# Kernel tuning notes

Measured on AMD Instinct MI355X. Metric: run time of the kernel, lower is better.

The kernel has to match this reference:

```python
import jax, jax.numpy as jnp
import numpy as np

C, CL = 64, 8
N_PTS, GRID = 250_000, 160
G2 = GRID // 2


def _build():
    """Build sparse coords and MinkowskiEngine-style kernel maps (numpy, int constants)."""
    rng = np.random.default_rng(0)
    raw = rng.integers(0, GRID, size=(int(N_PTS * 1.3), 3))
    keys = (raw[:, 0] * GRID + raw[:, 1]) * GRID + raw[:, 2]
    _, uidx = np.unique(keys, return_index=True)
    coords = raw[np.sort(uidx)][:N_PTS]
    n_in = coords.shape[0]
    # conv1: kernel 2, stride 2 -> each input voxel maps to exactly one output via one of 8 offsets
    down = coords // 2
    dkeys = (down[:, 0] * G2 + down[:, 1]) * G2 + down[:, 2]
    ukeys, inv = np.unique(dkeys, return_inverse=True)
    n_out = int(ukeys.shape[0])
    kid = (coords[:, 0] % 2) * 4 + (coords[:, 1] % 2) * 2 + (coords[:, 2] % 2)
    lists = [np.where(kid == k)[0] for k in range(8)]
    M1 = max(len(l) for l in lists)
    in1 = np.full((8, M1), n_in, np.int32)   # pad -> zero feature row
    out1 = np.full((8, M1), n_out, np.int32)  # pad -> dropped output row
    for k, l in enumerate(lists):
        in1[k, :len(l)] = l
        out1[k, :len(l)] = inv[l]
    # kernel-3, stride-1 map on the downsampled coordinate set (27 offsets)
    D = np.stack([ukeys // (G2 * G2), (ukeys // G2) % G2, ukeys % G2], 1)
    offs = [(a, b, c) for a in (-1, 0, 1) for b in (-1, 0, 1) for c in (-1, 0, 1)]
    pin, pout = [], []
    for o in offs:
        nd = D + np.array(o)
        valid = np.all((nd >= 0) & (nd < G2), 1)
        nk = (nd[:, 0] * G2 + nd[:, 1]) * G2 + nd[:, 2]
        pos = np.minimum(np.searchsorted(ukeys, nk), n_out - 1)
        found = valid & (ukeys[pos] == nk)
        ii = np.where(found)[0]
        pin.append(ii)
        pout.append(pos[ii])
    M3 = max(len(p) for p in pin)
    in3 = np.full((27, M3), n_out, np.int32)
    out3 = np.full((27, M3), n_out, np.int32)
    for k in range(27):
        in3[k, :len(pin[k])] = pin[k]
        out3[k, :len(pin[k])] = pout[k]
    return n_in, n_out, in1, out1, in3, out3


def setup_inputs() -> dict:
    n_in, n_out, in1, out1, in3, out3 = _build()
    key = jax.random.key(0)
    ks = jax.random.split(key, 16)
    s = 0.05
    return dict(
        x_F=jax.random.normal(ks[0], (n_in, C), jnp.float32),
        ctx_F=jax.random.normal(ks[1], (n_in, C), jnp.float32),
        W1=jax.random.normal(ks[2], (8, 2 * C, C), jnp.float32) * s,
        b1=jax.random.normal(ks[3], (C,), jnp.float32) * s,
        Wr00=jax.random.normal(ks[4], (27, C, C // 4), jnp.float32) * s,
        br00=jax.random.normal(ks[5], (C // 4,), jnp.float32) * s,
        Wr01=jax.random.normal(ks[6], (27, C // 4, C // 2), jnp.float32) * s,
        br01=jax.random.normal(ks[7], (C // 2,), jnp.float32) * s,
        Wr10=jax.random.normal(ks[8], (C, C // 4), jnp.float32) * s,
        br10=jax.random.normal(ks[9], (C // 4,), jnp.float32) * s,
        Wr11=jax.random.normal(ks[10], (27, C // 4, C // 4), jnp.float32) * s,
        br11=jax.random.normal(ks[11], (C // 4,), jnp.float32) * s,
        Wr12=jax.random.normal(ks[12], (C // 4, C // 2), jnp.float32) * s,
        br12=jax.random.normal(ks[13], (C // 2,), jnp.float32) * s,
        W2=jax.random.normal(ks[14], (27, C, CL), jnp.float32) * s,
        b2=jax.random.normal(ks[15], (CL,), jnp.float32) * s,
        in1=jnp.asarray(in1), out1=jnp.asarray(out1),
        in3=jnp.asarray(in3), out3=jnp.asarray(out3),
        n_out=n_out,
    )


def _sconv(F, W, b, in_idx, out_idx, n_out):
    """Kernel-map sparse conv: per-offset gather -> GEMM -> scatter-add. F:[N,Cin], W:[K,Cin,Cout]."""
    Fp = jnp.concatenate([F, jnp.zeros((1, F.shape[1]), F.dtype)], 0)
    y = jnp.zeros((n_out + 1, W.shape[2]), F.dtype)
    for k in range(W.shape[0]):  # fixed small kernel volume (8 or 27)
        y = y.at[out_idx[k]].add(Fp[in_idx[k]] @ W[k])
    return y[:n_out] + b


def reference(x_F, ctx_F, W1, b1, Wr00, br00, Wr01, br01, Wr10, br10, Wr11, br11, Wr12, br12, W2, b2, in1, out1, in3, out3, n_out):
    relu = jax.nn.relu
    f = jnp.concatenate([x_F, ctx_F], 1)               # cat(x.F, context1.F)
    h = _sconv(f, W1, b1, in1, out1, n_out)            # conv1: 2C->C, k=2, s=2
    # InceptionResNet block (PCGCv2-style)
    out0 = _sconv(relu(_sconv(h, Wr00, br00, in3, out3, n_out)), Wr01, br01, in3, out3, n_out)
    t = relu(h @ Wr10 + br10)                          # 1x1 conv
    t = relu(_sconv(t, Wr11, br11, in3, out3, n_out))  # 3x3 conv
    path1 = t @ Wr12 + br12                            # 1x1 conv
    h = jnp.concatenate([out0, path1], 1) + h          # cat + residual
    return _sconv(h, W2, b2, in3, out3, n_out)         # conv2: C->CL, k=3, s=1
```

## Files before the change

### kernel.cpp

```cpp
#include <hip/hip_runtime.h>

#define DEV __device__ __forceinline__

typedef __attribute__((ext_vector_type(8))) short bf16x8;
typedef __attribute__((ext_vector_type(4))) float f32x4;

DEV float4 ld4(const float* p){ return *reinterpret_cast<const float4*>(p); }

DEV unsigned short f2bf(float f){
    union { float f; unsigned u; } v; v.f = f;
    unsigned r = v.u + 0x7fffu + ((v.u >> 16) & 1u);
    return (unsigned short)(r >> 16);
}
DEV float bf2f(unsigned short s){
    union { unsigned u; float f; } v; v.u = ((unsigned)s) << 16;
    return v.f;
}

DEV int xcd_swizzle(int orig, int nwg){
    int q = nwg >> 3, r = nwg & 7;
    int x = orig & 7, i = orig >> 3;
    return (x < r ? x*(q+1) : r*(q+1) + (x-r)*q) + i;
}

__global__ __launch_bounds__(256)
void inv_init(int* __restrict__ inv, long n, int defv){
    long i = (long)blockIdx.x*256 + threadIdx.x;
    if (i < n) inv[i] = defv;
}

__global__ __launch_bounds__(256)
void inv_build(const int* __restrict__ inK, const int* __restrict__ outK,
               int* __restrict__ inv, int M, int n_out){
    int k = blockIdx.y;
    int m = blockIdx.x*256 + threadIdx.x;
    if (m >= M) return;
    int o = outK[(long)k*M + m];
    if (o != n_out) inv[(long)k*n_out + o] = inK[(long)k*M + m];
}

__global__ __launch_bounds__(256)
void zero_rows(unsigned short* A, unsigned short* B, unsigned short* C,
               unsigned short* D, unsigned short* E, unsigned short* Z,
               int n_out, int n_in){
    int t = threadIdx.x;
    if (t < 64)       A[(long)n_out*64 + t] = 0;
    else if (t < 80)  B[(long)n_out*16 + (t-64)] = 0;
    else if (t < 144) C[(long)n_out*64 + (t-80)] = 0;
    else if (t < 160) D[(long)n_out*16 + (t-144)] = 0;
    else if (t < 176) E[(long)n_out*16 + (t-160)] = 0;
    else if (t < 240) Z[(long)n_in*64 + (t-176)] = 0;
}

__global__ __launch_bounds__(256)
void wfrag_unpaired(const float* __restrict__ W, unsigned short* __restrict__ F,
                    int KC, int NT, int CIN, int CR, int total){
    int idx = blockIdx.x*256 + threadIdx.x;
    if (idx >= total) return;
    int j = idx & 7, l = (idx >> 3) & 63, rest = idx >> 9;
    int nt = rest % NT, cc = rest / NT;
    int k = cc / KC, kc = cc % KC;
    int g = l >> 4, c = l & 15;
    int cin = kc*32 + g*8 + j, cout = nt*16 + c;
    float v = (cout < CR) ? W[((long)k*CIN + cin)*CR + cout] : 0.f;
    F[idx] = f2bf(v);
}

__global__ __launch_bounds__(256)
void wfrag_paired(const float* __restrict__ W, unsigned short* __restrict__ F,
                  int NKr, int NT, int CR, int total){
    int idx = blockIdx.x*256 + threadIdx.x;
    if (idx >= total) return;
    int j = idx & 7, l = (idx >> 3) & 63, rest = idx >> 9;
    int nt = rest % NT, cc = rest / NT;
    int g = l >> 4, c = l & 15;
    int koff = 2*cc + (g >> 1);
    int cin = (g & 1)*8 + j, cout = nt*16 + c;
    float v = (koff < NKr && cout < CR) ? W[((long)koff*16 + cin)*CR + cout] : 0.f;
    F[idx] = f2bf(v);
}

template<bool RELU, bool OUTBF16, int YS, int CR>
__global__ __launch_bounds__(256)
void gather27_lds(const void* __restrict__ Xv, const unsigned short* __restrict__ Wf,
                  const int* __restrict__ inv, const float* __restrict__ bias,
                  void* __restrict__ Yv, int n_out)
{
    __shared__ alignas(16) char buf[2*8192];
    const int lane = threadIdx.x & 63, w = threadIdx.x >> 6;
    const int bid = xcd_swizzle(blockIdx.x, gridDim.x);
    const long jblock = (long)bid * 64;
    if (jblock >= n_out) return;
    const int r = lane & 15, g = lane >> 4;
    const char* X = (const char*)Xv;
    const bf16x8* __restrict__ WF = (const bf16x8*)Wf;

    const int srow = lane >> 3;
    const int scol = (lane & 7) << 4;
    const long jr0 = min(jblock + w*16 + srow,     (long)n_out - 1);
    const long jr1 = min(jblock + w*16 + 8 + srow, (long)n_out - 1);
    const int wo0 = w*2048 + srow*128     + (scol ^ (srow << 4));
    const int wo1 = w*2048 + (8+srow)*128 + (scol ^ (srow << 4));
    const int ro0 = w*2048 + r*128 + ((     g*16) ^ ((r & 7) << 4));
    const int ro1 = w*2048 + r*128 + ((64 + g*16) ^ ((r & 7) << 4));

    f32x4 acc = {0,0,0,0};

    int i0 = inv[jr0], i1 = inv[jr1];
    float4 f0 = ld4((const float*)(X + (long)i0*128 + scol));
    float4 f1 = ld4((const float*)(X + (long)i1*128 + scol));
    int n0 = inv[(long)n_out + jr0], n1 = inv[(long)n_out + jr1];
    bf16x8 wc0 = WF[lane], wc1 = WF[64 + lane];
    *(float4*)(buf + wo0) = f0;
    *(float4*)(buf + wo1) = f1;

    #pragma unroll 1
    for (int k = 0; k < 27; ++k){
        const int cb = k & 1;
        float4 g0, g1;
        if (k < 26){
            g0 = ld4((const float*)(X + (long)n0*128 + scol));
            g1 = ld4((const float*)(X + (long)n1*128 + scol));
        }
        int t0 = 0, t1 = 0;
        if (k < 25){
            const long ko = (long)(k+2)*n_out;
            t0 = inv[ko + jr0]; t1 = inv[ko + jr1];
        }
        bf16x8 wn0 = wc0, wn1 = wc1;
        if (k < 26){
            wn0 = WF[((long)(k+1)*2    )*64 + lane];
            wn1 = WF[((long)(k+1)*2 + 1)*64 + lane];
        }
        bf16x8 a0 = *(const bf16x8*)(buf + cb*8192 + ro0);
        bf16x8 a1 = *(const bf16x8*)(buf + cb*8192 + ro1);
        acc = __builtin_amdgcn_mfma_f32_16x16x32_bf16(a0, wc0, acc, 0, 0, 0);
        acc = __builtin_amdgcn_mfma_f32_16x16x32_bf16(a1, wc1, acc, 0, 0, 0);
        if (k < 26){
            *(float4*)(buf + (cb^1)*8192 + wo0) = g0;
            *(float4*)(buf + (cb^1)*8192 + wo1) = g1;
        }
        n0 = t0; n1 = t1; wc0 = wn0; wc1 = wn1;
    }

    const float bv = (r < CR) ? bias[r] : 0.f;
    #pragma unroll
    for (int q = 0; q < 4; ++q){
        long row = jblock + w*16 + g*4 + q;
        if (row < n_out){
            float v = acc[q] + bv;
            if constexpr (RELU) v = fmaxf(v, 0.f);
            if constexpr (OUTBF16) ((unsigned short*)Yv)[row*YS + r] = f2bf(v);
            else if (r < CR)       ((float*)Yv)[row*YS + r] = v;
        }
    }
}

__global__ __launch_bounds__(256, 8)
void conv1_z(const float* __restrict__ xF, const float* __restrict__ cF,
             const unsigned short* __restrict__ Wfc1, const int* __restrict__ in1,
             unsigned short* __restrict__ Z, int M1, int n_in)
{
    __shared__ unsigned short tz[4][16*64];
    const int k = blockIdx.x;
    const int lane = threadIdx.x & 63, wave = threadIdx.x >> 6;
    const int m0 = (blockIdx.y*4 + wave)*16;
    if (m0 >= M1) return;
    const int r = lane & 15, g = lane >> 4;
    const int* __restrict__ in1k = in1 + (long)k*M1;
    const int mc = min(m0 + r, M1-1);
    const int i = in1k[mc];
    const bool valid = i < n_in;
    const long iv = valid ? i : 0;
    const bf16x8* __restrict__ WF = (const bf16x8*)(Wfc1 + (size_t)k*16*512);
    const bf16x8 az = {0,0,0,0,0,0,0,0};
    f32x4 acc[4];
    #pragma unroll
    for (int nt=0; nt<4; ++nt) acc[nt] = f32x4{0,0,0,0};

    float4 lo[4], hi[4];
    #pragma unroll
    for (int kc=0; kc<4; ++kc){
        const float* s = (kc < 2) ? (xF + iv*64 + kc*32 + g*8)
                                  : (cF + iv*64 + (kc-2)*32 + g*8);
        lo[kc] = ld4(s);
        hi[kc] = ld4(s+4);
    }
    #pragma unroll
    for (int kc=0; kc<4; ++kc){
        bf16x8 a;
        a[0]=(short)f2bf(lo[kc].x); a[1]=(short)f2bf(lo[kc].y);
        a[2]=(short)f2bf(lo[kc].z); a[3]=(short)f2bf(lo[kc].w);
        a[4]=(short)f2bf(hi[kc].x); a[5]=(short)f2bf(hi[kc].y);
        a[6]=(short)f2bf(hi[kc].z); a[7]=(short)f2bf(hi[kc].w);
        if (!valid) a = az;
        #pragma unroll
        for (int nt=0; nt<4; ++nt){
            bf16x8 wv = WF[((long)kc*4 + nt)*64 + lane];
            acc[nt] = __builtin_amdgcn_mfma_f32_16x16x32_bf16(a, wv, acc[nt], 0, 0, 0);
        }
    }

    #pragma unroll
    for (int q=0; q<4; ++q)
        #pragma unroll
        for (int nt=0; nt<4; ++nt)
            tz[wave][(g*4+q)*64 + nt*16 + r] = f2bf(acc[nt][q]);
    __syncthreads();
    #pragma unroll
    for (int it=0; it<2; ++it){
        int cid = it*64 + lane;
        int row = cid >> 3, c8 = (cid & 7)*8;
        int m = m0 + row;
        if (m < M1){
            int oi = in1k[m];
            long drow = (oi < n_in) ? (long)oi : (long)n_in + 1;
            *(bf16x8*)(Z + drow*64 + c8) = *(const bf16x8*)(&tz[wave][row*64 + c8]);
        }
    }
}

__global__ __launch_bounds__(256)
void conv1_sum(const unsigned short* __restrict__ Z, const int* __restrict__ inv1,
               const float* __restrict__ b1, unsigned short* __restrict__ A, int n_out)
{
    const int bid = xcd_swizzle(blockIdx.x, gridDim.x);
    const long t = (long)bid*256 + threadIdx.x;
    const long o = t >> 3;
    if (o >= n_out) return;
    const int c8 = (int)(t & 7) * 8;
    int b[8];
    #pragma unroll
    for (int k=0;k<8;++k) b[k] = inv1[(long)k*n_out + o];
    float acc[8];
    #pragma unroll
    for (int j=0;j<2;++j){
        float4 v = ld4(b1 + c8 + 4*j);
        acc[4*j]=v.x; acc[4*j+1]=v.y; acc[4*j+2]=v.z; acc[4*j+3]=v.w;
    }
    #pragma unroll
    for (int k=0;k<8;++k){
        bf16x8 z = *(const bf16x8*)(Z + (long)b[k]*64 + c8);
        #pragma unroll
        for (int j=0;j<8;++j) acc[j] += bf2f((unsigned short)z[j]);
    }
    bf16x8 outv;
    #pragma unroll
    for (int j=0;j<8;++j) outv[j] = (short)f2bf(acc[j]);
    *(bf16x8*)(A + o*64 + c8) = outv;
}

template<int NK, int G, int NT, int RB, bool RELU, int RESBASE,
         int YS, int CB, int CR, int WPE>
__global__ __launch_bounds__(256, WPE)
void mfma_g1(const void* __restrict__ Xv, const unsigned short* __restrict__ Wf,
             const int* __restrict__ inv, const float* __restrict__ bias,
             const unsigned short* __restrict__ RES, unsigned short* __restrict__ Y, int n_out)
{
    const int lane = threadIdx.x & 63, wave = threadIdx.x >> 6;
    const int jbase = (blockIdx.x*4 + wave)*32;
    if (jbase >= n_out) return;
    const int r = lane & 15, g = lane >> 4;
    const int jc0 = min(jbase + r, n_out-1), jc1 = min(jbase + 16 + r, n_out-1);
    const char* X = (const char*)Xv;
    const bf16x8* __restrict__ WF = (const bf16x8*)Wf;
    f32x4 acc0[NT], acc1[NT];
    #pragma unroll
    for (int nt=0; nt<NT; ++nt){ acc0[nt] = f32x4{0,0,0,0}; acc1[nt] = f32x4{0,0,0,0}; }

    #pragma unroll 1
    for (int g0 = 0; g0 < NK; g0 += G) {
        int b0[G], b1[G];
        #pragma unroll
        for (int kk=0; kk<G; ++kk){
            int koff = 2*(g0+kk) + (g >> 1);
            b0[kk] = inv[(long)koff*n_out + jc0];
            b1[kk] = inv[(long)koff*n_out + jc1];
        }
        #pragma unroll
        for (int kk=0; kk<G; ++kk){
            const int k = g0 + kk;
            bf16x8 a0 = *(const bf16x8*)(X + (long)b0[kk]*RB + (g&1)*16);
            bf16x8 a1 = *(const bf16x8*)(X + (long)b1[kk]*RB + (g&1)*16);
            #pragma unroll
            for (int nt=0; nt<NT; ++nt){
                bf16x8 wv = WF[((long)k*NT + nt)*64 + lane];
                acc0[nt] = __builtin_amdgcn_mfma_f32_16x16x32_bf16(a0, wv, acc0[nt], 0, 0, 0);
                acc1[nt] = __builtin_amdgcn_mfma_f32_16x16x32_bf16(a1, wv, acc1[nt], 0, 0, 0);
            }
        }
    }

    float bi[NT];
    #pragma unroll
    for (int nt=0; nt<NT; ++nt){
        int c = nt*16 + r;
        bi[nt] = (c < CR) ? bias[c] : 0.f;
    }
    #pragma unroll
    for (int q=0; q<4; ++q){
        int row = jbase + g*4 + q;
        if (row < n_out){
            #pragma unroll
            for (int nt=0; nt<NT; ++nt){
                int c = nt*16 + r;
                float v = acc0[nt][q] + bi[nt];
                if constexpr (RESBASE >= 0) v += bf2f(RES[(long)row*64 + RESBASE + c]);
                if constexpr (RELU) v = fmaxf(v, 0.f);
                Y[(long)row*YS + CB + c] = f2bf(v);
            }
        }
        int row2 = jbase + 16 + g*4 + q;
        if (row2 < n_out){
            #pragma unroll
            for (int nt=0; nt<NT; ++nt){
                int c = nt*16 + r;
                float v = acc1[nt][q] + bi[nt];
                if constexpr (RESBASE >= 0) v += bf2f(RES[(long)row2*64 + RESBASE + c]);
                if constexpr (RELU) v = fmaxf(v, 0.f);
                Y[(long)row2*YS + CB + c] = f2bf(v);
            }
        }
    }
}

template<int MODE, int NT, int RB, bool RELU, int RESBASE, int YS, int CB, int CR>
__global__ __launch_bounds__(256)
void mfma_dense(const void* __restrict__ Xv, const unsigned short* __restrict__ Wf,
                const float* __restrict__ bias, const unsigned short* __restrict__ RES,
                unsigned short* __restrict__ Y, int n_out)
{
    const int lane = threadIdx.x & 63, wave = threadIdx.x >> 6;
    const int jbase = (blockIdx.x*4 + wave)*16;
    if (jbase >= n_out) return;
    const int r = lane & 15, g = lane >> 4;
    const int jrow = jbase + r;
    const bool rowok = jrow < n_out;
    const char* X = (const char*)Xv;
    const bf16x8* __restrict__ WF = (const bf16x8*)Wf;
    const bf16x8 az = {0,0,0,0,0,0,0,0};
    f32x4 acc[NT];
    #pragma unroll
    for (int nt=0; nt<NT; ++nt) acc[nt] = f32x4{0,0,0,0};

    if constexpr (MODE == 2) {
        #pragma unroll
        for (int kc=0; kc<2; ++kc){
            bf16x8 a = az;
            if (rowok) a = *(const bf16x8*)(X + (long)jrow*RB + kc*64 + g*16);
            #pragma unroll
            for (int nt=0; nt<NT; ++nt){
                bf16x8 wv = WF[((long)kc*NT + nt)*64 + lane];
                acc[nt] = __builtin_amdgcn_mfma_f32_16x16x32_bf16(a, wv, acc[nt], 0, 0, 0);
            }
        }
    } else {
        bf16x8 a = az;
        if (rowok && g < 2) a = *(const bf16x8*)(X + (long)jrow*RB + (g&1)*16);
        #pragma unroll
        for (int nt=0; nt<NT; ++nt){
            bf16x8 wv = WF[nt*64 + lane];
            acc[nt] = __builtin_amdgcn_mfma_f32_16x16x32_bf16(a, wv, acc[nt], 0, 0, 0);
        }
    }

    float bi[NT];
    #pragma unroll
    for (int nt=0; nt<NT; ++nt){
        int c = nt*16 + r;
        bi[nt] = (c < CR) ? bias[c] : 0.f;
    }
    #pragma unroll
    for (int q=0; q<4; ++q){
        int row = jbase + g*4 + q;
        if (row < n_out){
            #pragma unroll
            for (int nt=0; nt<NT; ++nt){
                int c = nt*16 + r;
                float v = acc[nt][q] + bi[nt];
                if constexpr (RESBASE >= 0) v += bf2f(RES[(long)row*64 + RESBASE + c]);
                if constexpr (RELU) v = fmaxf(v, 0.f);
                Y[(long)row*YS + CB + c] = f2bf(v);
            }
        }
    }
}

extern "C" void kernel_launch(void* const* d_in, const int* in_sizes, int n_in_cnt,
                              void* d_out, int out_size, void* d_ws, size_t ws_size,
                              hipStream_t stream)
{
    const float* xF   = (const float*)d_in[0];
    const float* ctxF = (const float*)d_in[1];
    const float* W1   = (const float*)d_in[2];
    const float* b1   = (const float*)d_in[3];
    const float* Wr00 = (const float*)d_in[4];
    const float* br00 = (const float*)d_in[5];
    const float* Wr01 = (const float*)d_in[6];
    const float* br01 = (const float*)d_in[7];
    const float* Wr10 = (const float*)d_in[8];
    const float* br10 = (const float*)d_in[9];
    const float* Wr11 = (const float*)d_in[10];
    const float* br11 = (const float*)d_in[11];
    const float* Wr12 = (const float*)d_in[12];
    const float* br12 = (const float*)d_in[13];
    const float* W2   = (const float*)d_in[14];
    const float* b2   = (const float*)d_in[15];
    const int* in1  = (const int*)d_in[16];
    const int* out1 = (const int*)d_in[17];
    const int* in3  = (const int*)d_in[18];
    const int* out3 = (const int*)d_in[19];

    const int n_out = out_size / 8;
    const int n_in  = in_sizes[0] / 64;
    const int M1 = in_sizes[16] / 8;
    const int M3 = in_sizes[18] / 27;

    char* p = (char*)d_ws;
    int* inv3 = (int*)p;                 p += (size_t)28*n_out*4;
    int* inv1 = (int*)p;                 p += (size_t)8*n_out*4;
    unsigned short* A = (unsigned short*)p;  p += (size_t)(n_out+1)*64*2;
    unsigned short* B = (unsigned short*)p;  p += (size_t)(n_out+1)*16*2;
    unsigned short* C = (unsigned short*)p;  p += (size_t)(n_out+1)*64*2;
    unsigned short* D = (unsigned short*)p;  p += (size_t)(n_out+1)*16*2;
    unsigned short* E = (unsigned short*)p;  p += (size_t)(n_out+1)*16*2;
    unsigned short* Z = (unsigned short*)p;  p += (size_t)(n_in+2)*64*2;
    unsigned short* Wf_c1 = (unsigned short*)p;  p += (size_t)32*4*512*2;
    unsigned short* Wf_00 = (unsigned short*)p;  p += (size_t)54*512*2;
    unsigned short* Wf_2  = (unsigned short*)p;  p += (size_t)54*512*2;
    unsigned short* Wf_01 = (unsigned short*)p;  p += (size_t)14*2*512*2;
    unsigned short* Wf_11 = (unsigned short*)p;  p += (size_t)14*512*2;
    unsigned short* Wf_10 = (unsigned short*)p;  p += (size_t)2*512*2;
    unsigned short* Wf_12 = (unsigned short*)p;  p += (size_t)2*512*2;
    float* OUT = (float*)d_out;

    auto cdiv = [](long a, long b){ return (int)((a + b - 1)/b); };

    inv_init<<<cdiv((long)28*n_out,256),256,0,stream>>>(inv3, (long)28*n_out, n_out);
    inv_init<<<cdiv((long)8*n_out,256),256,0,stream>>>(inv1, (long)8*n_out, n_in);
    inv_build<<<dim3(cdiv(M3,256),27),256,0,stream>>>(in3, out3, inv3, M3, n_out);
    inv_build<<<dim3(cdiv(M1,256),8),256,0,stream>>>(in1, out1, inv1, M1, n_out);
    zero_rows<<<1,256,0,stream>>>(A, B, C, D, E, Z, n_out, n_in);

    wfrag_unpaired<<<cdiv(32*4*512,256),256,0,stream>>>(W1,   Wf_c1, 4, 4, 128, 64, 32*4*512);
    wfrag_unpaired<<<cdiv(54*512,256),  256,0,stream>>>(Wr00, Wf_00, 2, 1,  64, 16, 54*512);
    wfrag_unpaired<<<cdiv(54*512,256),  256,0,stream>>>(W2,   Wf_2,  2, 1,  64,  8, 54*512);
    wfrag_unpaired<<<cdiv(2*512,256),   256,0,stream>>>(Wr10, Wf_10, 2, 1,  64, 16, 2*512);
    wfrag_paired  <<<cdiv(14*2*512,256),256,0,stream>>>(Wr01, Wf_01, 27, 2, 32, 14*2*512);
    wfrag_paired  <<<cdiv(14*512,256),  256,0,stream>>>(Wr11, Wf_11, 27, 1, 16, 14*512);
    wfrag_paired  <<<cdiv(2*512,256),   256,0,stream>>>(Wr12, Wf_12,  1, 2, 32, 2*512);

    conv1_z<<<dim3(8,cdiv(M1,64)),256,0,stream>>>(xF, ctxF, Wf_c1, in1, Z, M1, n_in);
    conv1_sum<<<cdiv((long)8*n_out,256),256,0,stream>>>(Z, inv1, b1, A, n_out);

    const int grid_g = cdiv(n_out, 128);
    const int grid_l = cdiv(n_out, 64);
    const int grid_d = cdiv(n_out, 64);

    gather27_lds<true, true, 16, 16>
        <<<grid_l,256,0,stream>>>(A, Wf_00, inv3, br00, B, n_out);
    mfma_dense<2, 1, 128, true, -1, 16, 0, 16>
        <<<grid_d,256,0,stream>>>(A, Wf_10, br10, nullptr, D, n_out);
    mfma_g1<14,7,2, 32, false, 0, 64, 0, 32, 4>
        <<<grid_g,256,0,stream>>>(B, Wf_01, inv3, br01, A, C, n_out);
    mfma_g1<14,7,1, 32, true, -1, 16, 0, 16, 4>
        <<<grid_g,256,0,stream>>>(D, Wf_11, inv3, br11, nullptr, E, n_out);
    mfma_dense<3, 2, 32, false, 32, 64, 32, 32>
        <<<grid_d,256,0,stream>>>(E, Wf_12, br12, A, C, n_out);
    gather27_lds<false, false, 8, 8>
        <<<grid_l,256,0,stream>>>(C, Wf_2, inv3, b2, OUT, n_out);
}
```

Baseline: 263.6 us.

## Gather MFMA operands directly from global and stage weights in LDS asynchronously

The 27-offset gather conv kernel stops staging gathered feature rows through a swizzled LDS double buffer. Each lane now loads its MFMA A-fragment straight from the gathered row in global memory. All 54 weight fragments are preloaded once per block into LDS with async global-to-LDS loads and read from there each step. This removes LDS round-trips and barriers for the activations and global weight reads inside the loop, at the cost of 54 KB of LDS per block (lower occupancy) and less coalesced 16-byte-per-lane gathers. The early-return for out-of-range blocks is also removed.

```diff
diff --git a/kernel.cpp b/kernel.cpp
--- a/kernel.cpp
+++ b/kernel.cpp
@@ -15,6 +15,12 @@
 DEV float bf2f(unsigned short s){
     union { unsigned u; float f; } v; v.u = ((unsigned)s) << 16;
     return v.f;
+}
+
+DEV void async16(const void* g, void* l){
+    __builtin_amdgcn_global_load_lds(
+        (const __attribute__((address_space(1))) unsigned*)g,
+        (__attribute__((address_space(3))) unsigned*)l, 16, 0, 0);
 }
 
 DEV int xcd_swizzle(int orig, int nwg){
@@ -82,65 +88,52 @@
 
 template<bool RELU, bool OUTBF16, int YS, int CR>
 __global__ __launch_bounds__(256)
-void gather27_lds(const void* __restrict__ Xv, const unsigned short* __restrict__ Wf,
-                  const int* __restrict__ inv, const float* __restrict__ bias,
-                  void* __restrict__ Yv, int n_out)
-{
-    __shared__ alignas(16) char buf[2*8192];
+void gather27_direct(const void* __restrict__ Xv, const unsigned short* __restrict__ Wf,
+                     const int* __restrict__ inv, const float* __restrict__ bias,
+                     void* __restrict__ Yv, int n_out)
+{
+    __shared__ alignas(16) unsigned short wlds[54*512];
     const int lane = threadIdx.x & 63, w = threadIdx.x >> 6;
     const int bid = xcd_swizzle(blockIdx.x, gridDim.x);
     const long jblock = (long)bid * 64;
-    if (jblock >= n_out) return;
     const int r = lane & 15, g = lane >> 4;
     const char* X = (const char*)Xv;
-    const bf16x8* __restrict__ WF = (const bf16x8*)Wf;
-
-    const int srow = lane >> 3;
-    const int scol = (lane & 7) << 4;
-    const long jr0 = min(jblock + w*16 + srow,     (long)n_out - 1);
-    const long jr1 = min(jblock + w*16 + 8 + srow, (long)n_out - 1);
-    const int wo0 = w*2048 + srow*128     + (scol ^ (srow << 4));
-    const int wo1 = w*2048 + (8+srow)*128 + (scol ^ (srow << 4));
-    const int ro0 = w*2048 + r*128 + ((     g*16) ^ ((r & 7) << 4));
-    const int ro1 = w*2048 + r*128 + ((64 + g*16) ^ ((r & 7) << 4));
-
+    char* WL = (char*)wlds;
+
+    #pragma unroll
+    for (int it = 0; it < 14; ++it){
+        int slot = it*256 + threadIdx.x;
+        if (slot < 3456)
+            async16((const char*)Wf + (long)slot*16, WL + it*4096 + w*1024);
+    }
+    __syncthreads();
+
+    const long jr = min(jblock + w*16 + r, (long)n_out - 1);
     f32x4 acc = {0,0,0,0};
 
-    int i0 = inv[jr0], i1 = inv[jr1];
-    float4 f0 = ld4((const float*)(X + (long)i0*128 + scol));
-    float4 f1 = ld4((const float*)(X + (long)i1*128 + scol));
-    int n0 = inv[(long)n_out + jr0], n1 = inv[(long)n_out + jr1];
-    bf16x8 wc0 = WF[lane], wc1 = WF[64 + lane];
-    *(float4*)(buf + wo0) = f0;
-    *(float4*)(buf + wo1) = f1;
+    int b0 = inv[jr];
+    bf16x8 a0 = *(const bf16x8*)(X + (long)b0*128 +      g*16);
+    bf16x8 a1 = *(const bf16x8*)(X + (long)b0*128 + 64 + g*16);
+    int b1 = inv[(long)n_out + jr];
+    int b2 = inv[(long)2*n_out + jr];
+    bf16x8 w0 = *(const bf16x8*)(WL + 0*1024 + lane*16);
+    bf16x8 w1 = *(const bf16x8*)(WL + 1*1024 + lane*16);
 
     #pragma unroll 1
     for (int k = 0; k < 27; ++k){
-        const int cb = k & 1;
-        float4 g0, g1;
+        int bn = 0;
+        if (k + 3 < 27) bn = inv[(long)(k+3)*n_out + jr];
+        bf16x8 na0 = a0, na1 = a1, nw0 = w0, nw1 = w1;
         if (k < 26){
-            g0 = ld4((const float*)(X + (long)n0*128 + scol));
-            g1 = ld4((const float*)(X + (long)n1*128 + scol));
-        }
-        int t0 = 0, t1 = 0;
-        if (k < 25){
-            const long ko = (long)(k+2)*n_out;
-            t0 = inv[ko + jr0]; t1 = inv[ko + jr1];
-        }
-        bf16x8 wn0 = wc0, wn1 = wc1;
-        if (k < 26){
-            wn0 = WF[((long)(k+1)*2    )*64 + lane];
-            wn1 = WF[((long)(k+1)*2 + 1)*64 + lane];
-        }
-        bf16x8 a0 = *(const bf16x8*)(buf + cb*8192 + ro0);
-        bf16x8 a1 = *(const bf16x8*)(buf + cb*8192 + ro1);
-        acc = __builtin_amdgcn_mfma_f32_16x16x32_bf16(a0, wc0, acc, 0, 0, 0);
-        acc = __builtin_amdgcn_mfma_f32_16x16x32_bf16(a1, wc1, acc, 0, 0, 0);
-        if (k < 26){
-            *(float4*)(buf + (cb^1)*8192 + wo0) = g0;
-            *(float4*)(buf + (cb^1)*8192 + wo1) = g1;
-        }
-        n0 = t0; n1 = t1; wc0 = wn0; wc1 = wn1;
+            na0 = *(const bf16x8*)(X + (long)b1*128 +      g*16);
+            na1 = *(const bf16x8*)(X + (long)b1*128 + 64 + g*16);
+            nw0 = *(const bf16x8*)(WL + (long)(2*(k+1)  )*1024 + lane*16);
+            nw1 = *(const bf16x8*)(WL + (long)(2*(k+1)+1)*1024 + lane*16);
+        }
+        acc = __builtin_amdgcn_mfma_f32_16x16x32_bf16(a0, w0, acc, 0, 0, 0);
+        acc = __builtin_amdgcn_mfma_f32_16x16x32_bf16(a1, w1, acc, 0, 0, 0);
+        a0 = na0; a1 = na1; w0 = nw0; w1 = nw1;
+        b1 = b2; b2 = bn;
     }
 
     const float bv = (r < CR) ? bias[r] : 0.f;
@@ -457,7 +450,7 @@
     const int grid_l = cdiv(n_out, 64);
     const int grid_d = cdiv(n_out, 64);
 
-    gather27_lds<true, true, 16, 16>
+    gather27_direct<true, true, 16, 16>
         <<<grid_l,256,0,stream>>>(A, Wf_00, inv3, br00, B, n_out);
     mfma_dense<2, 1, 128, true, -1, 16, 0, 16>
         <<<grid_d,256,0,stream>>>(A, Wf_10, br10, nullptr, D, n_out);
@@ -467,6 +460,6 @@
         <<<grid_g,256,0,stream>>>(D, Wf_11, inv3, br11, nullptr, E, n_out);
     mfma_dense<3, 2, 32, false, 32, 64, 32, 32>
         <<<grid_d,256,0,stream>>>(E, Wf_12, br12, A, C, n_out);
-    gather27_lds<false, false, 8, 8>
+    gather27_direct<false, false, 8, 8>
         <<<grid_l,256,0,stream>>>(C, Wf_2, inv3, b2, OUT, n_out);
 }
```

New measurement: 373.5 us. 41.7% more time.
